# Kernel optimization log

Measured on AMD Instinct MI355X. Metric: run time of the kernel, lower is better.

## Reference

```python
import jax, jax.numpy as jnp
import numpy as np

N, E, IN, D, H, G = 10000, 320000, 256, 128, 4, 64


def setup_inputs() -> dict:
    key = jax.random.key(0)
    ks = jax.random.split(key, 16)
    s = 0.05
    x = jax.random.normal(ks[0], (N, IN), jnp.float32)
    W1s = jax.random.normal(ks[1], (IN, H * D), jnp.float32) * s
    b1s = jnp.zeros((H * D,), jnp.float32)
    W1d = jax.random.normal(ks[2], (IN, H * D), jnp.float32) * s
    b1d = jnp.zeros((H * D,), jnp.float32)
    attn1 = jax.random.normal(ks[3], (H, D), jnp.float32) * s
    W2s = jax.random.normal(ks[4], (H * D, D), jnp.float32) * s
    b2s = jnp.zeros((D,), jnp.float32)
    W2d = jax.random.normal(ks[5], (H * D, D), jnp.float32) * s
    b2d = jnp.zeros((D,), jnp.float32)
    attn2 = jax.random.normal(ks[6], (1, D), jnp.float32) * s
    Wr1 = jax.random.normal(ks[7], (D, 64), jnp.float32) * s
    br1 = jnp.zeros((64,), jnp.float32)
    Wr2 = jax.random.normal(ks[8], (64, 1), jnp.float32) * s
    br2 = jnp.zeros((1,), jnp.float32)
    src = jax.random.randint(ks[9], (E,), 0, N)
    dst = jax.random.randint(ks[10], (E,), 0, N)
    # batched-graph node->graph assignment (contiguous, like dgl.batch)
    graph_ids = (jnp.arange(N) * G) // N
    return dict(x=x, W1s=W1s, b1s=b1s, W1d=W1d, b1d=b1d, attn1=attn1,
                W2s=W2s, b2s=b2s, W2d=W2d, b2d=b2d, attn2=attn2,
                Wr1=Wr1, br1=br1, Wr2=Wr2, br2=br2,
                src=src, dst=dst, graph_ids=graph_ids, num_graphs=G)


def gatv2_layer(x, Ws, bs, Wd, bd, attn, src, dst, n):
    """DGL GATv2Conv: e = a . leaky_relu(W_s x_u + W_d x_v), softmax over dst."""
    heads = attn.shape[0]
    hs = (x @ Ws + bs).reshape(n, heads, -1)   # [N,H,D] source projection
    hd = (x @ Wd + bd).reshape(n, heads, -1)   # [N,H,D] dest projection
    e = jax.nn.leaky_relu(hs[src] + hd[dst], negative_slope=0.2)  # [E,H,D]
    score = jnp.einsum('ehd,hd->eh', e, attn)  # [E,H]
    m = jax.ops.segment_max(score, dst, num_segments=n)           # [N,H]
    ex = jnp.exp(score - m[dst])
    denom = jax.ops.segment_sum(ex, dst, num_segments=n)
    alpha = ex / denom[dst]                                       # [E,H]
    out = jax.ops.segment_sum(alpha[:, :, None] * hs[src], dst, num_segments=n)
    return out  # [N,H,D]


def reference(x, W1s, b1s, W1d, b1d, attn1, W2s, b2s, W2d, b2d, attn2,
              Wr1, br1, Wr2, br2, src, dst, graph_ids, num_graphs):
    n = x.shape[0]
    h = gatv2_layer(x, W1s, b1s, W1d, b1d, attn1, src, dst, n).reshape(n, -1)  # [N,H*D]
    h = gatv2_layer(h, W2s, b2s, W2d, b2d, attn2, src, dst, n).mean(axis=1)    # [N,D]
    counts = jax.ops.segment_sum(jnp.ones((n,), h.dtype), graph_ids, num_segments=num_graphs)
    hg = jax.ops.segment_sum(h, graph_ids, num_segments=num_graphs) / jnp.maximum(counts, 1.0)[:, None]
    out = jax.nn.relu(hg @ Wr1 + br1) @ Wr2 + br2  # [G,1]
    return out.squeeze(-1)
```

## Files before the change

kernel.cpp:

```cpp
#include <hip/hip_runtime.h>

typedef __attribute__((ext_vector_type(8))) short bf16x8;
typedef __attribute__((ext_vector_type(4))) float f32x4;

#define N_NODES 10000
#define N_EDGES 320000
#define DIM_IN  256
#define DD      128
#define HH      4
#define HD      512
#define GG      64

__global__ void hist_kernel(const int* __restrict__ dst, int* __restrict__ cnt) {
  int e = blockIdx.x * 256 + threadIdx.x;
  atomicAdd(&cnt[dst[e]], 1);
}

__global__ void scan_kernel(const int* __restrict__ cnt, int* __restrict__ row_off) {
  __shared__ int part[1024];
  int t = threadIdx.x;
  int base = t * 10;
  int s = 0;
#pragma unroll
  for (int i = 0; i < 10; i++) { int idx = base + i; if (idx < N_NODES) s += cnt[idx]; }
  part[t] = s;
  __syncthreads();
  for (int off = 1; off < 1024; off <<= 1) {
    int v = (t >= off) ? part[t - off] : 0;
    __syncthreads();
    part[t] += v;
    __syncthreads();
  }
  int run = part[t] - s;
  for (int i = 0; i < 10; i++) {
    int idx = base + i;
    if (idx < N_NODES) { row_off[idx] = run; run += cnt[idx]; }
  }
  if (t == 1023) row_off[N_NODES] = part[1023];
}

__global__ void scatter_kernel(const int* __restrict__ src, const int* __restrict__ dst,
                               const int* __restrict__ row_off,
                               int* __restrict__ fill, int* __restrict__ srcl) {
  int e = blockIdx.x * 256 + threadIdx.x;
  int d = dst[e];
  int pos = row_off[d] + atomicAdd(&fill[d], 1);
  srcl[pos] = src[e];
}

__device__ inline void split4(float4 v, ushort4& h, ushort4& l) {
  uint bx = __float_as_uint(v.x), by = __float_as_uint(v.y);
  uint bz = __float_as_uint(v.z), bw = __float_as_uint(v.w);
  float rx = v.x - __uint_as_float(bx & 0xFFFF0000u);
  float ry = v.y - __uint_as_float(by & 0xFFFF0000u);
  float rz = v.z - __uint_as_float(bz & 0xFFFF0000u);
  float rw = v.w - __uint_as_float(bw & 0xFFFF0000u);
  h.x = (unsigned short)(bx >> 16); h.y = (unsigned short)(by >> 16);
  h.z = (unsigned short)(bz >> 16); h.w = (unsigned short)(bw >> 16);
  l.x = (unsigned short)(__float_as_uint(rx) >> 16);
  l.y = (unsigned short)(__float_as_uint(ry) >> 16);
  l.z = (unsigned short)(__float_as_uint(rz) >> 16);
  l.w = (unsigned short)(__float_as_uint(rw) >> 16);
}

__global__ __launch_bounds__(256) void split_rm(const float* __restrict__ in,
                                                ushort* __restrict__ oh,
                                                ushort* __restrict__ ol, int n4) {
  int i = blockIdx.x * 256 + threadIdx.x;
  if (i >= n4) return;
  float4 v = ((const float4*)in)[i];
  ushort4 h, l;
  split4(v, h, l);
  ((ushort4*)oh)[i] = h;
  ((ushort4*)ol)[i] = l;
}

__global__ __launch_bounds__(256) void split_tr2(
    const float* __restrict__ in0, ushort* __restrict__ oh0, ushort* __restrict__ ol0,
    const float* __restrict__ in1, ushort* __restrict__ oh1, ushort* __restrict__ ol1,
    int K, int N, int lgN) {
  const float* in = blockIdx.y ? in1 : in0;
  ushort* oh = blockIdx.y ? oh1 : oh0;
  ushort* ol = blockIdx.y ? ol1 : ol0;
  int id = blockIdx.x * 256 + threadIdx.x;
  int n = id & (N - 1);
  int kq = id >> lgN;
  if (kq >= (K >> 2)) return;
  int k = kq * 4;
  float4 v;
  v.x = in[(size_t)(k + 0) * N + n];
  v.y = in[(size_t)(k + 1) * N + n];
  v.z = in[(size_t)(k + 2) * N + n];
  v.w = in[(size_t)(k + 3) * N + n];
  ushort4 h, l;
  split4(v, h, l);
  *(ushort4*)(oh + (size_t)n * K + k) = h;
  *(ushort4*)(ol + (size_t)n * K + k) = l;
}

template <int K, int NCOL>
__global__ __launch_bounds__(256) void dual_gemm_mfma(
    const ushort* __restrict__ Ahg, const ushort* __restrict__ Alg,
    const ushort* __restrict__ B1hg, const ushort* __restrict__ B1lg,
    const float* __restrict__ bias1,
    const ushort* __restrict__ B2hg, const ushort* __restrict__ B2lg,
    const float* __restrict__ bias2,
    float* __restrict__ C1, float* __restrict__ C2, int M) {
  __shared__ ushort Ah[64][40], Al[64][40];
  __shared__ ushort B1h[64][40], B1l[64][40], B2h[64][40], B2l[64][40];
  int t = threadIdx.x;
  int lane = t & 63, wv = t >> 6;
  int wr = wv >> 1, wc = wv & 1;
  int l15 = lane & 15, l16 = lane >> 4;
  int col0 = blockIdx.x * 64, m0 = blockIdx.y * 64;

  int sr = t >> 2;
  int sk = (t & 3) * 8;
  bool arow_ok = (m0 + sr) < M;
  const ushort* pAh = Ahg + (size_t)(m0 + sr) * K + sk;
  const ushort* pAl = Alg + (size_t)(m0 + sr) * K + sk;
  const ushort* pB1h = B1hg + (size_t)(col0 + sr) * K + sk;
  const ushort* pB1l = B1lg + (size_t)(col0 + sr) * K + sk;
  const ushort* pB2h = B2hg + (size_t)(col0 + sr) * K + sk;
  const ushort* pB2l = B2lg + (size_t)(col0 + sr) * K + sk;

  f32x4 zero = {0.f, 0.f, 0.f, 0.f};
  f32x4 acc1[2][2], acc2[2][2];
#pragma unroll
  for (int i = 0; i < 2; i++)
#pragma unroll
    for (int j = 0; j < 2; j++) { acc1[i][j] = zero; acc2[i][j] = zero; }

  uint4 vah, val, v1h, v1l, v2h, v2l;
#define LOADK(KO)                                                            \
  vah = arow_ok ? *(const uint4*)(pAh + (KO)) : make_uint4(0u, 0u, 0u, 0u);  \
  val = arow_ok ? *(const uint4*)(pAl + (KO)) : make_uint4(0u, 0u, 0u, 0u);  \
  v1h = *(const uint4*)(pB1h + (KO));                                        \
  v1l = *(const uint4*)(pB1l + (KO));                                        \
  v2h = *(const uint4*)(pB2h + (KO));                                        \
  v2l = *(const uint4*)(pB2l + (KO));
  LOADK(0)
  for (int k0 = 0; k0 < K; k0 += 32) {
    __syncthreads();
    *(uint4*)&Ah[sr][sk] = vah;
    *(uint4*)&Al[sr][sk] = val;
    *(uint4*)&B1h[sr][sk] = v1h;
    *(uint4*)&B1l[sr][sk] = v1l;
    *(uint4*)&B2h[sr][sk] = v2h;
    *(uint4*)&B2l[sr][sk] = v2l;
    __syncthreads();
    if (k0 + 32 < K) { LOADK(k0 + 32) }
#pragma unroll
    for (int cb = 0; cb < 2; cb++) {
      int bc = wc * 32 + cb * 16 + l15;
      bf16x8 b1hf = *(const bf16x8*)&B1h[bc][l16 * 8];
      bf16x8 b1lf = *(const bf16x8*)&B1l[bc][l16 * 8];
      bf16x8 b2hf = *(const bf16x8*)&B2h[bc][l16 * 8];
      bf16x8 b2lf = *(const bf16x8*)&B2l[bc][l16 * 8];
#pragma unroll
      for (int rb = 0; rb < 2; rb++) {
        int arw = wr * 32 + rb * 16 + l15;
        bf16x8 ahf = *(const bf16x8*)&Ah[arw][l16 * 8];
        bf16x8 alf = *(const bf16x8*)&Al[arw][l16 * 8];
        acc1[rb][cb] = __builtin_amdgcn_mfma_f32_16x16x32_bf16(ahf, b1hf, acc1[rb][cb], 0, 0, 0);
        acc1[rb][cb] = __builtin_amdgcn_mfma_f32_16x16x32_bf16(ahf, b1lf, acc1[rb][cb], 0, 0, 0);
        acc1[rb][cb] = __builtin_amdgcn_mfma_f32_16x16x32_bf16(alf, b1hf, acc1[rb][cb], 0, 0, 0);
        acc2[rb][cb] = __builtin_amdgcn_mfma_f32_16x16x32_bf16(ahf, b2hf, acc2[rb][cb], 0, 0, 0);
        acc2[rb][cb] = __builtin_amdgcn_mfma_f32_16x16x32_bf16(ahf, b2lf, acc2[rb][cb], 0, 0, 0);
        acc2[rb][cb] = __builtin_amdgcn_mfma_f32_16x16x32_bf16(alf, b2hf, acc2[rb][cb], 0, 0, 0);
      }
    }
  }
#undef LOADK
#pragma unroll
  for (int rb = 0; rb < 2; rb++) {
#pragma unroll
    for (int cb = 0; cb < 2; cb++) {
      int row = m0 + wr * 32 + rb * 16 + l16 * 4;
      int col = col0 + wc * 32 + cb * 16 + l15;
      float bb1 = bias1[col], bb2 = bias2[col];
#pragma unroll
      for (int rr = 0; rr < 4; rr++) {
        if (row + rr < M) {
          C1[(size_t)(row + rr) * NCOL + col] = acc1[rb][cb][rr] + bb1;
          C2[(size_t)(row + rr) * NCOL + col] = acc2[rb][cb][rr] + bb2;
        }
      }
    }
  }
}

__global__ __launch_bounds__(256) void fused_gat1(
    const float* __restrict__ hs, const float* __restrict__ hd,
    const float* __restrict__ attn, const int* __restrict__ row_off,
    const int* __restrict__ srcl,
    ushort* __restrict__ outh, ushort* __restrict__ outl) {
  int t = threadIdx.x;
  int w = t >> 6, lane = t & 63;
  int slice = blockIdx.x & 3;
  int v = (blockIdx.x >> 2) * 4 + w;
  int off = slice * 128 + lane * 2;
  int start = row_off[v];
  int deg = row_off[v + 1] - start;

  float2 a = *(const float2*)(attn + off);
  float2 hdv = *(const float2*)(hd + (size_t)v * HD + off);
  const float* hsl = hs + off;

  float ssum = 0.f;
  float2 acc = make_float2(0.f, 0.f);

  for (int base = 0; base < deg; base += 64) {
    int nc = deg - base; nc = nc < 64 ? nc : 64;
    int myidx = (lane < nc) ? srcl[start + base + lane] : 0;

    float2 c0 = {0,0}, c1 = {0,0}, c2 = {0,0}, c3 = {0,0};
    if (0 < nc) c0 = *(const float2*)(hsl + (size_t)__builtin_amdgcn_readlane(myidx, 0) * HD);
    if (1 < nc) c1 = *(const float2*)(hsl + (size_t)__builtin_amdgcn_readlane(myidx, 1) * HD);
    if (2 < nc) c2 = *(const float2*)(hsl + (size_t)__builtin_amdgcn_readlane(myidx, 2) * HD);
    if (3 < nc) c3 = *(const float2*)(hsl + (size_t)__builtin_amdgcn_readlane(myidx, 3) * HD);

    for (int i0 = 0; i0 < nc; i0 += 4) {
#define GAT1_STEP(Q, C)                                                               \
      if (i0 + Q < nc) {                                                              \
        float2 u = C;                                                                 \
        int nx = i0 + 4 + Q;                                                          \
        if (nx < nc)                                                                  \
          C = *(const float2*)(hsl + (size_t)__builtin_amdgcn_readlane(myidx, nx) * HD); \
        float e0 = u.x + hdv.x; e0 = fmaxf(e0, 0.2f * e0);                            \
        float e1 = u.y + hdv.y; e1 = fmaxf(e1, 0.2f * e1);                            \
        float part = fmaf(e0, a.x, e1 * a.y);                                         \
        _Pragma("unroll")                                                             \
        for (int k = 1; k < 64; k <<= 1) part += __shfl_xor(part, k);                 \
        float wg = __expf(part);                                                      \
        ssum += wg;                                                                   \
        acc.x = fmaf(wg, u.x, acc.x);                                                 \
        acc.y = fmaf(wg, u.y, acc.y);                                                 \
      }
      GAT1_STEP(0, c0)
      GAT1_STEP(1, c1)
      GAT1_STEP(2, c2)
      GAT1_STEP(3, c3)
#undef GAT1_STEP
    }
  }
  float inv = ssum > 0.f ? 1.f / ssum : 0.f;
  float ox = acc.x * inv, oy = acc.y * inv;
  uint bx = __float_as_uint(ox), by = __float_as_uint(oy);
  float rx = ox - __uint_as_float(bx & 0xFFFF0000u);
  float ry = oy - __uint_as_float(by & 0xFFFF0000u);
  ushort2 hv, lv;
  hv.x = (unsigned short)(bx >> 16); hv.y = (unsigned short)(by >> 16);
  lv.x = (unsigned short)(__float_as_uint(rx) >> 16);
  lv.y = (unsigned short)(__float_as_uint(ry) >> 16);
  *(ushort2*)(outh + (size_t)v * HD + off) = hv;
  *(ushort2*)(outl + (size_t)v * HD + off) = lv;
}

__global__ __launch_bounds__(256) void fused_gat2(
    const float* __restrict__ hs, const float* __restrict__ hd,
    const float* __restrict__ attn, const int* __restrict__ row_off,
    const int* __restrict__ srcl, float* __restrict__ out) {
  int t = threadIdx.x;
  int w = t >> 6, lane = t & 63, grp = lane >> 4, sl = lane & 15;
  int v = blockIdx.x * 4 + w;
  int start = row_off[v];
  int deg = row_off[v + 1] - start;

  const float* ap = attn + sl * 8;
  const float* hp = hd + (size_t)v * DD + sl * 8;
  float4 a0 = *(const float4*)ap, a1 = *(const float4*)(ap + 4);
  float4 g0 = *(const float4*)hp, g1 = *(const float4*)(hp + 4);
  float areg[8] = {a0.x, a0.y, a0.z, a0.w, a1.x, a1.y, a1.z, a1.w};
  float hdreg[8] = {g0.x, g0.y, g0.z, g0.w, g1.x, g1.y, g1.z, g1.w};
  const float* hsl = hs + sl * 8;

  float ssum = 0.f;
  float acc[8] = {0.f, 0.f, 0.f, 0.f, 0.f, 0.f, 0.f, 0.f};

  float4 c0a = {0,0,0,0}, c0b = {0,0,0,0}, c1a = {0,0,0,0}, c1b = {0,0,0,0};
  if (grp < deg) { const float* p = hsl + (size_t)srcl[start + grp] * DD; c0a = *(const float4*)p; c0b = *(const float4*)(p + 4); }
  if (grp + 4 < deg) { const float* p = hsl + (size_t)srcl[start + grp + 4] * DD; c1a = *(const float4*)p; c1b = *(const float4*)(p + 4); }

  for (int i = grp; i < deg; i += 8) {
    float u0[8] = {c0a.x, c0a.y, c0a.z, c0a.w, c0b.x, c0b.y, c0b.z, c0b.w};
    float u1[8] = {c1a.x, c1a.y, c1a.z, c1a.w, c1b.x, c1b.y, c1b.z, c1b.w};
    bool have1 = (i + 4) < deg;
    if (i + 8 < deg) { const float* p = hsl + (size_t)srcl[start + i + 8] * DD; c0a = *(const float4*)p; c0b = *(const float4*)(p + 4); }
    if (i + 12 < deg) { const float* p = hsl + (size_t)srcl[start + i + 12] * DD; c1a = *(const float4*)p; c1b = *(const float4*)(p + 4); }
    float part0 = 0.f, part1 = 0.f;
#pragma unroll
    for (int j = 0; j < 8; j++) {
      float e0 = u0[j] + hdreg[j]; e0 = fmaxf(e0, 0.2f * e0);
      part0 = fmaf(e0, areg[j], part0);
      float e1 = u1[j] + hdreg[j]; e1 = fmaxf(e1, 0.2f * e1);
      part1 = fmaf(e1, areg[j], part1);
    }
#pragma unroll
    for (int k = 1; k < 16; k <<= 1) {
      part0 += __shfl_xor(part0, k);
      part1 += __shfl_xor(part1, k);
    }
    float wg0 = __expf(part0);
    float wg1 = have1 ? __expf(part1) : 0.f;
    ssum += wg0 + wg1;
#pragma unroll
    for (int j = 0; j < 8; j++)
      acc[j] = fmaf(wg0, u0[j], fmaf(wg1, u1[j], acc[j]));
  }
#pragma unroll
  for (int j = 0; j < 8; j++) {
    acc[j] += __shfl_xor(acc[j], 16);
    acc[j] += __shfl_xor(acc[j], 32);
  }
  ssum += __shfl_xor(ssum, 16);
  ssum += __shfl_xor(ssum, 32);
  float inv = ssum > 0.f ? 1.f / ssum : 0.f;
  if (lane < 16) {
    float* op = out + (size_t)v * DD + sl * 8;
    *(float4*)op = make_float4(acc[0] * inv, acc[1] * inv, acc[2] * inv, acc[3] * inv);
    *(float4*)(op + 4) = make_float4(acc[4] * inv, acc[5] * inv, acc[6] * inv, acc[7] * inv);
  }
}

__global__ __launch_bounds__(128) void final_kernel(
    const float* __restrict__ h2, const int* __restrict__ gid,
    const float* __restrict__ Wr1, const float* __restrict__ br1,
    const float* __restrict__ Wr2, const float* __restrict__ br2,
    float* __restrict__ out) {
  int g = blockIdx.x, t = threadIdx.x;
  int a, b;
  { int l = 0, h = N_NODES; while (l < h) { int m = (l + h) >> 1; if (gid[m] < g) l = m + 1; else h = m; } a = l; }
  { int l = a, h = N_NODES; while (l < h) { int m = (l + h) >> 1; if (gid[m] < g + 1) l = m + 1; else h = m; } b = l; }
  float s0 = 0.f, s1 = 0.f, s2 = 0.f, s3 = 0.f;
  int v = a;
  for (; v + 3 < b; v += 4) {
    s0 += h2[(size_t)(v + 0) * DD + t];
    s1 += h2[(size_t)(v + 1) * DD + t];
    s2 += h2[(size_t)(v + 2) * DD + t];
    s3 += h2[(size_t)(v + 3) * DD + t];
  }
  for (; v < b; v++) s0 += h2[(size_t)v * DD + t];
  __shared__ float hgn[128];
  float cnt = (float)(b - a);
  hgn[t] = ((s0 + s1) + (s2 + s3)) / fmaxf(cnt, 1.f);
  __syncthreads();
  if (t < 64) {
    float r = br1[t];
#pragma unroll 8
    for (int k = 0; k < 128; k++) r = fmaf(hgn[k], Wr1[k * 64 + t], r);
    r = fmaxf(r, 0.f);
    float p = r * Wr2[t];
#pragma unroll
    for (int k = 1; k < 64; k <<= 1) p += __shfl_xor(p, k);
    if (t == 0) out[g] = p + br2[0];
  }
}

extern "C" void kernel_launch(void* const* d_in, const int* in_sizes, int n_in,
                              void* d_out, int out_size, void* d_ws, size_t ws_size,
                              hipStream_t stream) {
  (void)in_sizes; (void)n_in; (void)out_size; (void)ws_size;
  const float* x     = (const float*)d_in[0];
  const float* W1s   = (const float*)d_in[1];
  const float* b1s   = (const float*)d_in[2];
  const float* W1d   = (const float*)d_in[3];
  const float* b1d   = (const float*)d_in[4];
  const float* attn1 = (const float*)d_in[5];
  const float* W2s   = (const float*)d_in[6];
  const float* b2s   = (const float*)d_in[7];
  const float* W2d   = (const float*)d_in[8];
  const float* b2d   = (const float*)d_in[9];
  const float* attn2 = (const float*)d_in[10];
  const float* Wr1   = (const float*)d_in[11];
  const float* br1   = (const float*)d_in[12];
  const float* Wr2   = (const float*)d_in[13];
  const float* br2   = (const float*)d_in[14];
  const int* src     = (const int*)d_in[15];
  const int* dst     = (const int*)d_in[16];
  const int* gid     = (const int*)d_in[17];
  float* out = (float*)d_out;

  char* ws = (char*)d_ws;
  float*  hs1     = (float*)(ws + 0);
  float*  hd1     = (float*)(ws + 20480000);
  ushort* h1h     = (ushort*)(ws + 40960000);
  ushort* h1l     = (ushort*)(ws + 51200000);
  ushort* xh      = (ushort*)(ws + 61440000);
  ushort* xl      = (ushort*)(ws + 66560000);
  int*    srcl    = (int*)(ws + 71680000);
  int*    row_off = (int*)(ws + 72960000);
  int*    cnt     = (int*)(ws + 73000064);
  int*    fill    = (int*)(ws + 73040064);
  ushort* b1sh    = (ushort*)(ws + 73080064);
  ushort* b1sl    = (ushort*)(ws + 73342208);
  ushort* b1dh    = (ushort*)(ws + 73604352);
  ushort* b1dl    = (ushort*)(ws + 73866496);
  ushort* b2sh    = (ushort*)(ws + 74128640);
  ushort* b2sl    = (ushort*)(ws + 74259712);
  ushort* b2dh    = (ushort*)(ws + 74390784);
  ushort* b2dl    = (ushort*)(ws + 74521856);
  float*  hs2     = (float*)(ws + 0);
  float*  hd2     = (float*)(ws + 5120000);
  float*  h2      = (float*)(ws + 40960000);

  hipMemsetAsync(cnt, 0, 2 * N_NODES * 4, stream);

  hist_kernel<<<N_EDGES / 256, 256, 0, stream>>>(dst, cnt);
  scan_kernel<<<1, 1024, 0, stream>>>(cnt, row_off);
  scatter_kernel<<<N_EDGES / 256, 256, 0, stream>>>(src, dst, row_off, fill, srcl);

  split_rm<<<(N_NODES * DIM_IN / 4 + 255) / 256, 256, 0, stream>>>(x, xh, xl, N_NODES * DIM_IN / 4);
  split_tr2<<<dim3((HD * (DIM_IN / 4) + 255) / 256, 2), 256, 0, stream>>>(
      W1s, b1sh, b1sl, W1d, b1dh, b1dl, DIM_IN, HD, 9);
  split_tr2<<<dim3((DD * (HD / 4) + 255) / 256, 2), 256, 0, stream>>>(
      W2s, b2sh, b2sl, W2d, b2dh, b2dl, HD, DD, 7);

  dual_gemm_mfma<DIM_IN, HD><<<dim3(HD / 64, (N_NODES + 63) / 64), 256, 0, stream>>>(
      xh, xl, b1sh, b1sl, b1s, b1dh, b1dl, b1d, hs1, hd1, N_NODES);
  fused_gat1<<<N_NODES, 256, 0, stream>>>(hs1, hd1, attn1, row_off, srcl, h1h, h1l);

  dual_gemm_mfma<HD, DD><<<dim3(DD / 64, (N_NODES + 63) / 64), 256, 0, stream>>>(
      h1h, h1l, b2sh, b2sl, b2s, b2dh, b2dl, b2d, hs2, hd2, N_NODES);
  fused_gat2<<<(N_NODES + 3) / 4, 256, 0, stream>>>(hs2, hd2, attn2, row_off, srcl, h2);

  final_kernel<<<GG, 128, 0, stream>>>(h2, gid, Wr1, br1, Wr2, br2, out);
}
```

Baseline: 248.9 us.

## Process two edges per wavefront in GAT layer-1 aggregation using half-wave float4 loads

```diff
diff --git a/kernel.cpp b/kernel.cpp
--- a/kernel.cpp
+++ b/kernel.cpp
@@ -199,43 +199,61 @@
   int w = t >> 6, lane = t & 63;
   int slice = blockIdx.x & 3;
   int v = (blockIdx.x >> 2) * 4 + w;
-  int off = slice * 128 + lane * 2;
+  int epar = lane >> 5;
+  int sl = lane & 31;
+  int off = slice * 128 + sl * 4;
   int start = row_off[v];
   int deg = row_off[v + 1] - start;
 
-  float2 a = *(const float2*)(attn + off);
-  float2 hdv = *(const float2*)(hd + (size_t)v * HD + off);
+  float4 a = *(const float4*)(attn + off);
+  float4 hdv = *(const float4*)(hd + (size_t)v * HD + off);
   const float* hsl = hs + off;
 
   float ssum = 0.f;
-  float2 acc = make_float2(0.f, 0.f);
+  float4 acc = make_float4(0.f, 0.f, 0.f, 0.f);
 
   for (int base = 0; base < deg; base += 64) {
     int nc = deg - base; nc = nc < 64 ? nc : 64;
     int myidx = (lane < nc) ? srcl[start + base + lane] : 0;
 
-    float2 c0 = {0,0}, c1 = {0,0}, c2 = {0,0}, c3 = {0,0};
-    if (0 < nc) c0 = *(const float2*)(hsl + (size_t)__builtin_amdgcn_readlane(myidx, 0) * HD);
-    if (1 < nc) c1 = *(const float2*)(hsl + (size_t)__builtin_amdgcn_readlane(myidx, 1) * HD);
-    if (2 < nc) c2 = *(const float2*)(hsl + (size_t)__builtin_amdgcn_readlane(myidx, 2) * HD);
-    if (3 < nc) c3 = *(const float2*)(hsl + (size_t)__builtin_amdgcn_readlane(myidx, 3) * HD);
-
-    for (int i0 = 0; i0 < nc; i0 += 4) {
+    float4 c0 = {0,0,0,0}, c1 = {0,0,0,0}, c2 = {0,0,0,0}, c3 = {0,0,0,0};
+#define GAT1_PRE(Q, C)                                                                \
+    { int iA = 2 * Q;                                                                 \
+      if (iA < nc) {                                                                  \
+        int iB = iA + 1;                                                              \
+        int idxA = __builtin_amdgcn_readlane(myidx, iA);                              \
+        int idxB = __builtin_amdgcn_readlane(myidx, iB < nc ? iB : iA);               \
+        int idx = epar ? idxB : idxA;                                                 \
+        C = *(const float4*)(hsl + (size_t)idx * HD); } }
+    GAT1_PRE(0, c0) GAT1_PRE(1, c1) GAT1_PRE(2, c2) GAT1_PRE(3, c3)
+#undef GAT1_PRE
+
+    for (int i0 = 0; i0 < nc; i0 += 8) {
 #define GAT1_STEP(Q, C)                                                               \
-      if (i0 + Q < nc) {                                                              \
-        float2 u = C;                                                                 \
-        int nx = i0 + 4 + Q;                                                          \
-        if (nx < nc)                                                                  \
-          C = *(const float2*)(hsl + (size_t)__builtin_amdgcn_readlane(myidx, nx) * HD); \
+      if (i0 + 2 * Q < nc) {                                                          \
+        float4 u = C;                                                                 \
+        int nA = i0 + 8 + 2 * Q;                                                      \
+        if (nA < nc) {                                                                \
+          int nB = nA + 1;                                                            \
+          int idxA = __builtin_amdgcn_readlane(myidx, nA);                            \
+          int idxB = __builtin_amdgcn_readlane(myidx, nB < nc ? nB : nA);             \
+          int idx = epar ? idxB : idxA;                                               \
+          C = *(const float4*)(hsl + (size_t)idx * HD);                               \
+        }                                                                             \
         float e0 = u.x + hdv.x; e0 = fmaxf(e0, 0.2f * e0);                            \
         float e1 = u.y + hdv.y; e1 = fmaxf(e1, 0.2f * e1);                            \
-        float part = fmaf(e0, a.x, e1 * a.y);                                         \
+        float e2 = u.z + hdv.z; e2 = fmaxf(e2, 0.2f * e2);                            \
+        float e3 = u.w + hdv.w; e3 = fmaxf(e3, 0.2f * e3);                            \
+        float part = fmaf(e0, a.x, fmaf(e1, a.y, fmaf(e2, a.z, e3 * a.w)));           \
         _Pragma("unroll")                                                             \
-        for (int k = 1; k < 64; k <<= 1) part += __shfl_xor(part, k);                 \
-        float wg = __expf(part);                                                      \
+        for (int k = 1; k < 32; k <<= 1) part += __shfl_xor(part, k);                 \
+        bool vld = (i0 + 2 * Q + epar) < nc;                                          \
+        float wg = vld ? __expf(part) : 0.f;                                          \
         ssum += wg;                                                                   \
         acc.x = fmaf(wg, u.x, acc.x);                                                 \
         acc.y = fmaf(wg, u.y, acc.y);                                                 \
+        acc.z = fmaf(wg, u.z, acc.z);                                                 \
+        acc.w = fmaf(wg, u.w, acc.w);                                                 \
       }
       GAT1_STEP(0, c0)
       GAT1_STEP(1, c1)
@@ -244,17 +262,19 @@
 #undef GAT1_STEP
     }
   }
-  float inv = ssum > 0.f ? 1.f / ssum : 0.f;
-  float ox = acc.x * inv, oy = acc.y * inv;
-  uint bx = __float_as_uint(ox), by = __float_as_uint(oy);
-  float rx = ox - __uint_as_float(bx & 0xFFFF0000u);
-  float ry = oy - __uint_as_float(by & 0xFFFF0000u);
-  ushort2 hv, lv;
-  hv.x = (unsigned short)(bx >> 16); hv.y = (unsigned short)(by >> 16);
-  lv.x = (unsigned short)(__float_as_uint(rx) >> 16);
-  lv.y = (unsigned short)(__float_as_uint(ry) >> 16);
-  *(ushort2*)(outh + (size_t)v * HD + off) = hv;
-  *(ushort2*)(outl + (size_t)v * HD + off) = lv;
+  acc.x += __shfl_xor(acc.x, 32);
+  acc.y += __shfl_xor(acc.y, 32);
+  acc.z += __shfl_xor(acc.z, 32);
+  acc.w += __shfl_xor(acc.w, 32);
+  ssum += __shfl_xor(ssum, 32);
+  if (lane < 32) {
+    float inv = ssum > 0.f ? 1.f / ssum : 0.f;
+    float4 o = make_float4(acc.x * inv, acc.y * inv, acc.z * inv, acc.w * inv);
+    ushort4 hv, lv;
+    split4(o, hv, lv);
+    *(ushort4*)(outh + (size_t)v * HD + off) = hv;
+    *(ushort4*)(outl + (size_t)v * HD + off) = lv;
+  }
 }
 
 __global__ __launch_bounds__(256) void fused_gat2(
```

Result: faster. 216.6 us (-13.0%).

## Process four edges per wavefront in gat1 with 16-lane groups and float4 loads

Applied to the files above, without the earlier changes.

```diff
diff --git a/kernel.cpp b/kernel.cpp
--- a/kernel.cpp
+++ b/kernel.cpp
@@ -199,62 +199,84 @@
   int w = t >> 6, lane = t & 63;
   int slice = blockIdx.x & 3;
   int v = (blockIdx.x >> 2) * 4 + w;
-  int off = slice * 128 + lane * 2;
+  int grp = lane >> 4, sl = lane & 15;
+  int off = slice * 128 + sl * 8;
   int start = row_off[v];
   int deg = row_off[v + 1] - start;
 
-  float2 a = *(const float2*)(attn + off);
-  float2 hdv = *(const float2*)(hd + (size_t)v * HD + off);
+  const float* ap = attn + off;
+  const float* hp = hd + (size_t)v * HD + off;
+  float4 a0 = *(const float4*)ap, a1 = *(const float4*)(ap + 4);
+  float4 g0 = *(const float4*)hp, g1 = *(const float4*)(hp + 4);
+  float areg[8] = {a0.x, a0.y, a0.z, a0.w, a1.x, a1.y, a1.z, a1.w};
+  float hdreg[8] = {g0.x, g0.y, g0.z, g0.w, g1.x, g1.y, g1.z, g1.w};
   const float* hsl = hs + off;
 
   float ssum = 0.f;
-  float2 acc = make_float2(0.f, 0.f);
+  float acc[8] = {0.f, 0.f, 0.f, 0.f, 0.f, 0.f, 0.f, 0.f};
 
   for (int base = 0; base < deg; base += 64) {
     int nc = deg - base; nc = nc < 64 ? nc : 64;
     int myidx = (lane < nc) ? srcl[start + base + lane] : 0;
 
-    float2 c0 = {0,0}, c1 = {0,0}, c2 = {0,0}, c3 = {0,0};
-    if (0 < nc) c0 = *(const float2*)(hsl + (size_t)__builtin_amdgcn_readlane(myidx, 0) * HD);
-    if (1 < nc) c1 = *(const float2*)(hsl + (size_t)__builtin_amdgcn_readlane(myidx, 1) * HD);
-    if (2 < nc) c2 = *(const float2*)(hsl + (size_t)__builtin_amdgcn_readlane(myidx, 2) * HD);
-    if (3 < nc) c3 = *(const float2*)(hsl + (size_t)__builtin_amdgcn_readlane(myidx, 3) * HD);
-
-    for (int i0 = 0; i0 < nc; i0 += 4) {
-#define GAT1_STEP(Q, C)                                                               \
-      if (i0 + Q < nc) {                                                              \
-        float2 u = C;                                                                 \
-        int nx = i0 + 4 + Q;                                                          \
-        if (nx < nc)                                                                  \
-          C = *(const float2*)(hsl + (size_t)__builtin_amdgcn_readlane(myidx, nx) * HD); \
-        float e0 = u.x + hdv.x; e0 = fmaxf(e0, 0.2f * e0);                            \
-        float e1 = u.y + hdv.y; e1 = fmaxf(e1, 0.2f * e1);                            \
-        float part = fmaf(e0, a.x, e1 * a.y);                                         \
-        _Pragma("unroll")                                                             \
-        for (int k = 1; k < 64; k <<= 1) part += __shfl_xor(part, k);                 \
-        float wg = __expf(part);                                                      \
-        ssum += wg;                                                                   \
-        acc.x = fmaf(wg, u.x, acc.x);                                                 \
-        acc.y = fmaf(wg, u.y, acc.y);                                                 \
+    float4 cAa = {0,0,0,0}, cAb = {0,0,0,0}, cBa = {0,0,0,0}, cBb = {0,0,0,0};
+    {
+      int eA = grp, eB = grp + 4;
+      int idxA = __shfl(myidx, eA < nc ? eA : 0);
+      int idxB = __shfl(myidx, eB < nc ? eB : 0);
+      if (eA < nc) { const float* p = hsl + (size_t)idxA * HD; cAa = *(const float4*)p; cAb = *(const float4*)(p + 4); }
+      if (eB < nc) { const float* p = hsl + (size_t)idxB * HD; cBa = *(const float4*)p; cBb = *(const float4*)(p + 4); }
+    }
+
+    for (int i0 = 0; i0 < nc; i0 += 8) {
+#define GAT1_STEP(S, CA, CB)                                                   \
+      { int e = i0 + 4 * S + grp;                                              \
+        int nx = i0 + 8 + 4 * S + grp;                                         \
+        int nidx = __shfl(myidx, nx < nc ? nx : 0);    \
+        bool vld = e < nc;                                                     \
+        float u[8] = {CA.x, CA.y, CA.z, CA.w, CB.x, CB.y, CB.z, CB.w};         \
+        if (nx < nc) {                                                         \
+          const float* p = hsl + (size_t)nidx * HD;                            \
+          CA = *(const float4*)p; CB = *(const float4*)(p + 4);                \
+        }                                                                      \
+        float part = 0.f;                                                      \
+        _Pragma("unroll")                                                      \
+        for (int j = 0; j < 8; j++) {                                          \
+          float ee = u[j] + hdreg[j];                                          \
+          ee = fmaxf(ee, 0.2f * ee);                                           \
+          part = fmaf(ee, areg[j], part);                                      \
+        }                                                                      \
+        _Pragma("unroll")                                                      \
+        for (int k = 1; k < 16; k <<= 1) part += __shfl_xor(part, k);          \
+        float wg = vld ? __expf(part) : 0.f;                                   \
+        ssum += wg;                                                            \
+        _Pragma("unroll")                                                      \
+        for (int j = 0; j < 8; j++) acc[j] = fmaf(wg, u[j], acc[j]);           \
       }
-      GAT1_STEP(0, c0)
-      GAT1_STEP(1, c1)
-      GAT1_STEP(2, c2)
-      GAT1_STEP(3, c3)
+      GAT1_STEP(0, cAa, cAb)
+      GAT1_STEP(1, cBa, cBb)
 #undef GAT1_STEP
     }
   }
-  float inv = ssum > 0.f ? 1.f / ssum : 0.f;
-  float ox = acc.x * inv, oy = acc.y * inv;
-  uint bx = __float_as_uint(ox), by = __float_as_uint(oy);
-  float rx = ox - __uint_as_float(bx & 0xFFFF0000u);
-  float ry = oy - __uint_as_float(by & 0xFFFF0000u);
-  ushort2 hv, lv;
-  hv.x = (unsigned short)(bx >> 16); hv.y = (unsigned short)(by >> 16);
-  lv.x = (unsigned short)(__float_as_uint(rx) >> 16);
-  lv.y = (unsigned short)(__float_as_uint(ry) >> 16);
-  *(ushort2*)(outh + (size_t)v * HD + off) = hv;
-  *(ushort2*)(outl + (size_t)v * HD + off) = lv;
+#pragma unroll
+  for (int j = 0; j < 8; j++) {
+    acc[j] += __shfl_xor(acc[j], 16);
+    acc[j] += __shfl_xor(acc[j], 32);
+  }
+  ssum += __shfl_xor(ssum, 16);
+  ssum += __shfl_xor(ssum, 32);
+  if (lane < 16) {
+    float inv = ssum > 0.f ? 1.f / ssum : 0.f;
+    float4 o0 = make_float4(acc[0] * inv, acc[1] * inv, acc[2] * inv, acc[3] * inv);
+    float4 o1 = make_float4(acc[4] * inv, acc[5] * inv, acc[6] * inv, acc[7] * inv);
+    ushort4 hv0, lv0, hv1, lv1;
+    split4(o0, hv0, lv0);
+    split4(o1, hv1, lv1);
+    *(ushort4*)(outh + (size_t)v * HD + off) = hv0;
+    *(ushort4*)(outh + (size_t)v * HD + off + 4) = hv1;
+    *(ushort4*)(outl + (size_t)v * HD + off) = lv0;
+    *(ushort4*)(outl + (size_t)v * HD + off + 4) = lv1;
+  }
 }
 
 __global__ __launch_bounds__(256) void fused_gat2(
```

Result: faster. 212.0 us (-14.8%).
